# Kernel optimization log

Hardware: AMD Instinct MI355X
Metric: run time of the kernel (lower is better)

## Reference

```python
import jax, jax.numpy as jnp
import numpy as np

# --- static hash-grid config (matches tcnn HashGrid in the torch module) ---
DIM = 3
N_LEVELS = 16
F = 2                      # n_features_per_level
LOG2_T = 19
T = 1 << LOG2_T            # hashmap size per level
BASE_RES = 16
TARGET_RES = 2048
PLS = float(np.exp2(np.log2(TARGET_RES / BASE_RES) / (N_LEVELS - 1)))  # per_level_scale
SCALES = [BASE_RES * PLS ** l for l in range(N_LEVELS)]
PRIMES = np.array([1, 2654435761, 805459861], dtype=np.uint32)
# 8 corner offsets of the unit cube, shape [8, 3]
OFFS = np.stack(np.meshgrid(*([np.arange(2)] * DIM), indexing='ij'), -1).reshape(-1, DIM).astype(np.float32)


def _hash(idx_u32):
    # idx_u32: [..., 3] uint32 -> [...] uint32 index into table of size T (power of 2)
    h = idx_u32[..., 0] * jnp.uint32(PRIMES[0])
    h = h ^ (idx_u32[..., 1] * jnp.uint32(PRIMES[1]))
    h = h ^ (idx_u32[..., 2] * jnp.uint32(PRIMES[2]))
    return h & jnp.uint32(T - 1)


def hashgrid_encode(x, table):
    # x: [N, 3] in [0,1); table: [L, T, F] fp32
    outs = []
    offs = jnp.asarray(OFFS)                      # [8, 3]
    for l in range(N_LEVELS):
        pos = x * jnp.float32(SCALES[l])          # [N, 3]
        base = jnp.floor(pos)
        frac = pos - base                         # [N, 3]
        corner = base[:, None, :] + offs[None]    # [N, 8, 3]
        idx = corner.astype(jnp.uint32)
        h = _hash(idx)                            # [N, 8]
        feat = table[l][h]                        # [N, 8, F] (gather)
        # trilinear weights: prod over dims of frac or (1-frac)
        w = jnp.prod(jnp.where(offs[None] > 0.5, frac[:, None, :], 1.0 - frac[:, None, :]), axis=-1)  # [N, 8]
        outs.append(jnp.sum(w[..., None] * feat, axis=1))  # [N, F]
    return jnp.concatenate(outs, axis=-1)         # [N, L*F] = [N, 32]


def setup_inputs() -> dict:
    key = jax.random.key(0)
    ks = jax.random.split(key, 8)
    N = 1048576
    dim_in = N_LEVELS * F          # 32
    hid = 16                       # (16+15)//16*16
    dout = 16                      # grid_output_dim
    x = jax.random.uniform(ks[0], (N, DIM), dtype=jnp.float32)
    table = jax.random.uniform(ks[1], (N_LEVELS, T, F), dtype=jnp.float32, minval=-1e-4, maxval=1e-4)
    def lin(k, fi, fo):
        b = 1.0 / np.sqrt(fi)
        return jax.random.uniform(k, (fo, fi), dtype=jnp.float32, minval=-b, maxval=b)
    W0 = lin(ks[2], dim_in, hid); b0 = jnp.zeros((hid,), jnp.float32)
    W1 = lin(ks[3], hid, hid);    b1 = jnp.zeros((hid,), jnp.float32)
    W2 = lin(ks[4], hid, dout);   b2 = jnp.zeros((dout,), jnp.float32)
    return {"x": x, "table": table, "W0": W0, "b0": b0, "W1": W1, "b1": b1, "W2": W2, "b2": b2}


def reference(x, table, W0, b0, W1, b1, W2, b2):
    h = hashgrid_encode(x, table)                 # [N, 32]
    h = jax.nn.relu(h @ W0.T + b0)
    h = jax.nn.relu(h @ W1.T + b1)
    return h @ W2.T + b2                          # [N, 16]
```

## Files before the change

### kernel.cpp

```cpp
#include <hip/hip_runtime.h>
#include <math.h>

#define NLV 16
#define LOG2_T 19
#define T_SIZE (1u << LOG2_T)
#define T_MASK (T_SIZE - 1u)
#define P2 2654435761u
#define P3 805459861u
#define NBUCK 32768

typedef float vf2 __attribute__((ext_vector_type(2)));
typedef float vf4 __attribute__((ext_vector_type(4)));

struct Scales { float s[NLV]; };

__device__ __forceinline__ unsigned mpart(unsigned v) {
    v = (v | (v << 8)) & 0x100Fu;
    v = (v | (v << 4)) & 0x10C3u;
    v = (v | (v << 2)) & 0x1249u;
    return v;
}
__device__ __forceinline__ unsigned mkey(float px, float py, float pz) {
    unsigned cx = (unsigned)(px * 32.f); cx = cx > 31u ? 31u : cx;
    unsigned cy = (unsigned)(py * 32.f); cy = cy > 31u ? 31u : cy;
    unsigned cz = (unsigned)(pz * 32.f); cz = cz > 31u ? 31u : cz;
    return mpart(cx) | (mpart(cy) << 1) | (mpart(cz) << 2);
}

__global__ __launch_bounds__(256) void zero_hist_kernel(unsigned* hist) {
    int i = blockIdx.x * 256 + threadIdx.x;
    if (i < NBUCK) hist[i] = 0u;
}

__global__ __launch_bounds__(256) void hist_kernel(
    const float* __restrict__ x, unsigned* __restrict__ hist, int N)
{
    const int q = blockIdx.x * 256 + threadIdx.x;
    const int i0 = q * 4;
    if (i0 >= N) return;
    if (i0 + 3 < N) {
        const vf4 A = *(const vf4*)(x + 12 * (size_t)q);
        const vf4 B = *(const vf4*)(x + 12 * (size_t)q + 4);
        const vf4 C = *(const vf4*)(x + 12 * (size_t)q + 8);
        const float px[4] = {A[0], A[3], B[2], C[1]};
        const float py[4] = {A[1], B[0], B[3], C[2]};
        const float pz[4] = {A[2], B[1], C[0], C[3]};
        #pragma unroll
        for (int k = 0; k < 4; ++k) atomicAdd(&hist[mkey(px[k], py[k], pz[k])], 1u);
    } else {
        for (int i = i0; i < N; ++i)
            atomicAdd(&hist[mkey(x[3*(size_t)i], x[3*(size_t)i+1], x[3*(size_t)i+2])], 1u);
    }
}

__global__ __launch_bounds__(1024) void scan_kernel(unsigned* hist) {
    __shared__ unsigned tot[1024];
    const int t = threadIdx.x;
    const unsigned base = (unsigned)t * 32u;
    unsigned loc[32];
    unsigned s = 0;
    #pragma unroll
    for (int k = 0; k < 32; ++k) { loc[k] = s; s += hist[base + k]; }
    tot[t] = s;
    __syncthreads();
    for (int off = 1; off < 1024; off <<= 1) {
        unsigned u = (t >= off) ? tot[t - off] : 0u;
        __syncthreads();
        tot[t] += u;
        __syncthreads();
    }
    const unsigned excl = tot[t] - s;
    #pragma unroll
    for (int k = 0; k < 32; ++k) hist[base + k] = excl + loc[k];
}

__global__ __launch_bounds__(256) void scatter_kernel(
    const float* __restrict__ x, unsigned* __restrict__ cursor,
    vf4* __restrict__ xs, int* __restrict__ perm, int N)
{
    const int q = blockIdx.x * 256 + threadIdx.x;
    const int i0 = q * 4;
    if (i0 >= N) return;
    if (i0 + 3 < N) {
        const vf4 A = *(const vf4*)(x + 12 * (size_t)q);
        const vf4 B = *(const vf4*)(x + 12 * (size_t)q + 4);
        const vf4 C = *(const vf4*)(x + 12 * (size_t)q + 8);
        const float px[4] = {A[0], A[3], B[2], C[1]};
        const float py[4] = {A[1], B[0], B[3], C[2]};
        const float pz[4] = {A[2], B[1], C[0], C[3]};
        #pragma unroll
        for (int k = 0; k < 4; ++k) {
            const unsigned key = mkey(px[k], py[k], pz[k]);
            const unsigned pos = atomicAdd(&cursor[key], 1u);
            vf4 v; v[0] = px[k]; v[1] = py[k]; v[2] = pz[k]; v[3] = 0.f;
            xs[pos] = v;
            perm[pos] = i0 + k;
        }
    } else {
        for (int i = i0; i < N; ++i) {
            const float px = x[3*(size_t)i], py = x[3*(size_t)i+1], pz = x[3*(size_t)i+2];
            const unsigned key = mkey(px, py, pz);
            const unsigned pos = atomicAdd(&cursor[key], 1u);
            vf4 v; v[0] = px; v[1] = py; v[2] = pz; v[3] = 0.f;
            xs[pos] = v;
            perm[pos] = i;
        }
    }
}

__device__ __forceinline__ void enc_level(
    float px, float py, float pz, float s, const float* __restrict__ tl,
    float& f0, float& f1)
{
    const float fx = px * s, fy = py * s, fz = pz * s;
    const float bx = floorf(fx), by = floorf(fy), bz = floorf(fz);
    const float rx = fx - bx, ry = fy - by, rz = fz - bz;
    const unsigned ix0 = (unsigned)bx, iy0 = (unsigned)by, iz0 = (unsigned)bz;
    const unsigned hx0 = ix0,      hx1 = ix0 + 1u;
    const unsigned hy0 = iy0 * P2, hy1 = (iy0 + 1u) * P2;
    const unsigned hz0 = iz0 * P3, hz1 = (iz0 + 1u) * P3;
    const float wx0 = 1.f - rx, wy0 = 1.f - ry, wz0 = 1.f - rz;
    f0 = 0.f; f1 = 0.f;
    #pragma unroll
    for (int c = 0; c < 8; ++c) {
        unsigned h = ((c & 4) ? hx1 : hx0) ^ ((c & 2) ? hy1 : hy0) ^ ((c & 1) ? hz1 : hz0);
        h &= T_MASK;
        const vf2 f = *(const vf2*)(tl + 2u * (size_t)h);
        const float w = ((c & 4) ? rx : wx0) * ((c & 2) ? ry : wy0) * ((c & 1) ? rz : wz0);
        f0 += w * f[0];
        f1 += w * f[1];
    }
}

__global__ __launch_bounds__(256) void encode_coarse_kernel(
    const vf4* __restrict__ xs, const float* __restrict__ table,
    float* __restrict__ enc, int N, Scales sc)
{
    int i = blockIdx.x * 256 + threadIdx.x;
    if (i >= N) return;
    const vf4 p = xs[i];
    #pragma unroll
    for (int l = 0; l < 5; ++l) {
        float f0, f1;
        enc_level(p[0], p[1], p[2], sc.s[l], table + (size_t)l * T_SIZE * 2u, f0, f1);
        vf2 v; v[0] = f0; v[1] = f1;
        *(vf2*)(enc + ((size_t)l * N + i) * 2u) = v;
    }
}

__global__ __launch_bounds__(256) void encode_one_kernel(
    const vf4* __restrict__ xs, const float* __restrict__ tl, float s,
    float* __restrict__ encl, int N)
{
    const int i0 = blockIdx.x * 1024 + threadIdx.x;
    #pragma unroll
    for (int k = 0; k < 4; ++k) {
        const int i = i0 + k * 256;
        if (i < N) {
            const vf4 p = xs[i];
            float f0, f1;
            enc_level(p[0], p[1], p[2], s, tl, f0, f1);
            vf2 v; v[0] = f0; v[1] = f1;
            *(vf2*)(encl + (size_t)i * 2u) = v;
        }
    }
}

__global__ __launch_bounds__(256) void mlp_kernel(
    const float* __restrict__ enc, const int* __restrict__ perm,
    const float* __restrict__ W0, const float* __restrict__ b0,
    const float* __restrict__ W1, const float* __restrict__ b1,
    const float* __restrict__ W2, const float* __restrict__ b2,
    float* __restrict__ out, int N)
{
    __shared__ float st[512 * 17];
    const int base = blockIdx.x * 512;
    const int t = threadIdx.x;
    const int p0 = base + 2 * t;

    if (p0 < N) {
        float e[64];
        #pragma unroll
        for (int l = 0; l < NLV; ++l) {
            vf4 v = *(const vf4*)(enc + ((size_t)l * N + p0) * 2u);
            e[4*l+0] = v[0]; e[4*l+1] = v[1]; e[4*l+2] = v[2]; e[4*l+3] = v[3];
        }
        #pragma unroll
        for (int q = 0; q < 2; ++q) {
            if (q == 0 || p0 + 1 < N) {
                float a0[16];
                #pragma unroll
                for (int j = 0; j < 16; ++j) {
                    float s = b0[j];
                    #pragma unroll
                    for (int l = 0; l < NLV; ++l) {
                        s += e[4*l + 2*q + 0] * W0[j * 32 + 2*l + 0];
                        s += e[4*l + 2*q + 1] * W0[j * 32 + 2*l + 1];
                    }
                    a0[j] = fmaxf(s, 0.f);
                }
                float a1[16];
                #pragma unroll
                for (int j = 0; j < 16; ++j) {
                    float s = b1[j];
                    #pragma unroll
                    for (int k = 0; k < 16; ++k) s += a0[k] * W1[j * 16 + k];
                    a1[j] = fmaxf(s, 0.f);
                }
                const int row = 2 * t + q;
                #pragma unroll
                for (int j = 0; j < 16; ++j) {
                    float s = b2[j];
                    #pragma unroll
                    for (int k = 0; k < 16; ++k) s += a1[k] * W2[j * 16 + k];
                    st[row * 17 + j] = s;
                }
            }
        }
    }
    __syncthreads();

    const int c = t & 3;
    #pragma unroll
    for (int w = 0; w < 8; ++w) {
        const int p = (t >> 2) + w * 64;
        const int gi = base + p;
        if (gi < N) {
            const int dst = perm[gi];
            const vf4 v = *(const vf4*)&st[p * 17 + 4 * c];
            *(vf4*)(out + 16 * (size_t)dst + 4 * c) = v;
        }
    }
}

__global__ __launch_bounds__(256) void encode_coarse_unsorted_kernel(
    const float* __restrict__ x, const float* __restrict__ table,
    float* __restrict__ enc, int N, Scales sc)
{
    int i = blockIdx.x * 256 + threadIdx.x;
    if (i >= N) return;
    const float px = x[3 * (size_t)i + 0];
    const float py = x[3 * (size_t)i + 1];
    const float pz = x[3 * (size_t)i + 2];
    #pragma unroll
    for (int l = 0; l < 5; ++l) {
        float f0, f1;
        enc_level(px, py, pz, sc.s[l], table + (size_t)l * T_SIZE * 2u, f0, f1);
        vf2 v; v[0] = f0; v[1] = f1;
        *(vf2*)(enc + ((size_t)l * N + i) * 2u) = v;
    }
}
__global__ __launch_bounds__(256) void encode_one_unsorted_kernel(
    const float* __restrict__ x, const float* __restrict__ tl, float s,
    float* __restrict__ encl, int N)
{
    int i = blockIdx.x * 256 + threadIdx.x;
    if (i >= N) return;
    const float px = x[3 * (size_t)i + 0];
    const float py = x[3 * (size_t)i + 1];
    const float pz = x[3 * (size_t)i + 2];
    float f0, f1;
    enc_level(px, py, pz, s, tl, f0, f1);
    vf2 v; v[0] = f0; v[1] = f1;
    *(vf2*)(encl + (size_t)i * 2u) = v;
}
__global__ __launch_bounds__(256) void mlp_noperm_kernel(
    const float* __restrict__ enc,
    const float* __restrict__ W0, const float* __restrict__ b0,
    const float* __restrict__ W1, const float* __restrict__ b1,
    const float* __restrict__ W2, const float* __restrict__ b2,
    float* __restrict__ out, int N)
{
    int i = blockIdx.x * 256 + threadIdx.x;
    if (i >= N) return;
    float e[32];
    #pragma unroll
    for (int l = 0; l < NLV; ++l) {
        vf2 v = *(const vf2*)(enc + ((size_t)l * N + i) * 2u);
        e[2 * l + 0] = v[0];
        e[2 * l + 1] = v[1];
    }
    float a0[16];
    #pragma unroll
    for (int j = 0; j < 16; ++j) {
        float s = b0[j];
        #pragma unroll
        for (int k = 0; k < 32; ++k) s += e[k] * W0[j * 32 + k];
        a0[j] = fmaxf(s, 0.f);
    }
    float a1[16];
    #pragma unroll
    for (int j = 0; j < 16; ++j) {
        float s = b1[j];
        #pragma unroll
        for (int k = 0; k < 16; ++k) s += a0[k] * W1[j * 16 + k];
        a1[j] = fmaxf(s, 0.f);
    }
    #pragma unroll
    for (int j = 0; j < 16; ++j) {
        float s = b2[j];
        #pragma unroll
        for (int k = 0; k < 16; ++k) s += a1[k] * W2[j * 16 + k];
        out[16 * (size_t)i + j] = s;
    }
}
__global__ __launch_bounds__(256) void tcnn_fused_kernel(
    const float* __restrict__ x, const float* __restrict__ table,
    const float* __restrict__ W0, const float* __restrict__ b0,
    const float* __restrict__ W1, const float* __restrict__ b1,
    const float* __restrict__ W2, const float* __restrict__ b2,
    float* __restrict__ out, int N, Scales sc)
{
    int i = blockIdx.x * blockDim.x + threadIdx.x;
    if (i >= N) return;
    const float px = x[3 * (size_t)i + 0];
    const float py = x[3 * (size_t)i + 1];
    const float pz = x[3 * (size_t)i + 2];
    float e[32];
    #pragma unroll
    for (int l = 0; l < NLV; ++l) {
        float f0, f1;
        enc_level(px, py, pz, sc.s[l], table + (size_t)l * T_SIZE * 2u, f0, f1);
        e[2 * l] = f0; e[2 * l + 1] = f1;
    }
    float a0[16];
    #pragma unroll
    for (int j = 0; j < 16; ++j) {
        float s = b0[j];
        #pragma unroll
        for (int k = 0; k < 32; ++k) s += e[k] * W0[j * 32 + k];
        a0[j] = fmaxf(s, 0.f);
    }
    float a1[16];
    #pragma unroll
    for (int j = 0; j < 16; ++j) {
        float s = b1[j];
        #pragma unroll
        for (int k = 0; k < 16; ++k) s += a0[k] * W1[j * 16 + k];
        a1[j] = fmaxf(s, 0.f);
    }
    #pragma unroll
    for (int j = 0; j < 16; ++j) {
        float s = b2[j];
        #pragma unroll
        for (int k = 0; k < 16; ++k) s += a1[k] * W2[j * 16 + k];
        out[16 * (size_t)i + j] = s;
    }
}

extern "C" void kernel_launch(void* const* d_in, const int* in_sizes, int n_in,
                              void* d_out, int out_size, void* d_ws, size_t ws_size,
                              hipStream_t stream) {
    const float* x     = (const float*)d_in[0];
    const float* table = (const float*)d_in[1];
    const float* W0    = (const float*)d_in[2];
    const float* b0    = (const float*)d_in[3];
    const float* W1    = (const float*)d_in[4];
    const float* b1    = (const float*)d_in[5];
    const float* W2    = (const float*)d_in[6];
    const float* b2    = (const float*)d_in[7];
    float* out = (float*)d_out;

    const int N = in_sizes[0] / 3;

    Scales sc;
    const double pls = exp2(log2(2048.0 / 16.0) / 15.0);
    for (int l = 0; l < NLV; ++l) sc.s[l] = (float)(16.0 * pow(pls, (double)l));

    const int block = 256;
    const int grid = (N + block - 1) / block;

    const size_t encB  = (size_t)N * 2u * NLV * sizeof(float);
    const size_t xsB   = (size_t)N * sizeof(float) * 4u;
    const size_t permB = (size_t)N * sizeof(int);
    const size_t histB = (size_t)NBUCK * sizeof(unsigned);

    if (ws_size >= encB + xsB + permB + histB) {
        float*    enc  = (float*)d_ws;
        vf4*      xs   = (vf4*)((char*)d_ws + encB);
        int*      perm = (int*)((char*)d_ws + encB + xsB);
        unsigned* hist = (unsigned*)((char*)d_ws + encB + xsB + permB);

        const int gridQ = (N + 1023) / 1024;
        zero_hist_kernel<<<(NBUCK + 255) / 256, block, 0, stream>>>(hist);
        hist_kernel<<<gridQ, block, 0, stream>>>(x, hist, N);
        scan_kernel<<<1, 1024, 0, stream>>>(hist);
        scatter_kernel<<<gridQ, block, 0, stream>>>(x, hist, xs, perm, N);

        encode_coarse_kernel<<<grid, block, 0, stream>>>(xs, table, enc, N, sc);
        for (int l = 5; l < NLV; ++l) {
            encode_one_kernel<<<gridQ, block, 0, stream>>>(
                xs, table + (size_t)l * T_SIZE * 2u, sc.s[l],
                enc + (size_t)l * (size_t)N * 2u, N);
        }
        const int gridM = (N + 511) / 512;
        mlp_kernel<<<gridM, block, 0, stream>>>(enc, perm, W0, b0, W1, b1, W2, b2, out, N);
    } else if (ws_size >= encB) {
        float* enc = (float*)d_ws;
        encode_coarse_unsorted_kernel<<<grid, block, 0, stream>>>(x, table, enc, N, sc);
        for (int l = 5; l < NLV; ++l) {
            encode_one_unsorted_kernel<<<grid, block, 0, stream>>>(
                x, table + (size_t)l * T_SIZE * 2u, sc.s[l],
                enc + (size_t)l * (size_t)N * 2u, N);
        }
        mlp_noperm_kernel<<<grid, block, 0, stream>>>(enc, W0, b0, W1, b1, W2, b2, out, N);
    } else {
        tcnn_fused_kernel<<<grid, block, 0, stream>>>(x, table, W0, b0, W1, b1, W2, b2,
                                                      out, N, sc);
    }
}
```

Before: 533.1 us.

## Use atomic relaxed loads for fine-level gathers and restructure MLP to halve LDS

For hash levels 8 and up, table gathers now use relaxed agent-scope atomic 64-bit loads, apparently to change the cache policy and avoid polluting caches with random, low-reuse accesses. Separately, the MLP kernel processes its 512 points in two passes of 256. Each pass uses a half-size shared staging buffer and vectorized float2 dot products. This lowers LDS use and register pressure at the cost of an extra barrier and store phase. The atomic-load codegen may behave differently from plain loads on this hardware.

After: 554.4 us. 1.04x slower.

```diff
diff --git a/kernel.cpp b/kernel.cpp
--- a/kernel.cpp
+++ b/kernel.cpp
@@ -108,7 +108,8 @@
     }
 }
 
-__device__ __forceinline__ void enc_level(
+template<bool BYPASS>
+__device__ __forceinline__ void enc_level_t(
     float px, float py, float pz, float s, const float* __restrict__ tl,
     float& f0, float& f1)
 {
@@ -125,7 +126,15 @@
     for (int c = 0; c < 8; ++c) {
         unsigned h = ((c & 4) ? hx1 : hx0) ^ ((c & 2) ? hy1 : hy0) ^ ((c & 1) ? hz1 : hz0);
         h &= T_MASK;
-        const vf2 f = *(const vf2*)(tl + 2u * (size_t)h);
+        vf2 f;
+        if constexpr (BYPASS) {
+            unsigned long long u = __hip_atomic_load(
+                (const unsigned long long*)(tl + 2u * (size_t)h),
+                __ATOMIC_RELAXED, __HIP_MEMORY_SCOPE_AGENT);
+            union { unsigned long long u; vf2 f; } cv; cv.u = u; f = cv.f;
+        } else {
+            f = *(const vf2*)(tl + 2u * (size_t)h);
+        }
         const float w = ((c & 4) ? rx : wx0) * ((c & 2) ? ry : wy0) * ((c & 1) ? rz : wz0);
         f0 += w * f[0];
         f1 += w * f[1];
@@ -142,12 +151,13 @@
     #pragma unroll
     for (int l = 0; l < 5; ++l) {
         float f0, f1;
-        enc_level(p[0], p[1], p[2], sc.s[l], table + (size_t)l * T_SIZE * 2u, f0, f1);
+        enc_level_t<false>(p[0], p[1], p[2], sc.s[l], table + (size_t)l * T_SIZE * 2u, f0, f1);
         vf2 v; v[0] = f0; v[1] = f1;
         *(vf2*)(enc + ((size_t)l * N + i) * 2u) = v;
     }
 }
 
+template<bool BYPASS>
 __global__ __launch_bounds__(256) void encode_one_kernel(
     const vf4* __restrict__ xs, const float* __restrict__ tl, float s,
     float* __restrict__ encl, int N)
@@ -159,7 +169,7 @@
         if (i < N) {
             const vf4 p = xs[i];
             float f0, f1;
-            enc_level(p[0], p[1], p[2], s, tl, f0, f1);
+            enc_level_t<BYPASS>(p[0], p[1], p[2], s, tl, f0, f1);
             vf2 v; v[0] = f0; v[1] = f1;
             *(vf2*)(encl + (size_t)i * 2u) = v;
         }
@@ -173,62 +183,59 @@
     const float* __restrict__ W2, const float* __restrict__ b2,
     float* __restrict__ out, int N)
 {
-    __shared__ float st[512 * 17];
+    __shared__ float st[256 * 17];
     const int base = blockIdx.x * 512;
     const int t = threadIdx.x;
-    const int p0 = base + 2 * t;
-
-    if (p0 < N) {
-        float e[64];
-        #pragma unroll
-        for (int l = 0; l < NLV; ++l) {
-            vf4 v = *(const vf4*)(enc + ((size_t)l * N + p0) * 2u);
-            e[4*l+0] = v[0]; e[4*l+1] = v[1]; e[4*l+2] = v[2]; e[4*l+3] = v[3];
-        }
-        #pragma unroll
-        for (int q = 0; q < 2; ++q) {
-            if (q == 0 || p0 + 1 < N) {
-                float a0[16];
+
+    #pragma unroll
+    for (int q = 0; q < 2; ++q) {
+        if (q) __syncthreads();
+        const int i = base + q * 256 + t;
+        if (i < N) {
+            vf2 e2[16];
+            #pragma unroll
+            for (int l = 0; l < NLV; ++l)
+                e2[l] = *(const vf2*)(enc + ((size_t)l * N + i) * 2u);
+
+            vf2 a0v[8];
+            #pragma unroll
+            for (int j = 0; j < 16; ++j) {
+                vf2 acc = {0.f, 0.f};
                 #pragma unroll
-                for (int j = 0; j < 16; ++j) {
-                    float s = b0[j];
-                    #pragma unroll
-                    for (int l = 0; l < NLV; ++l) {
-                        s += e[4*l + 2*q + 0] * W0[j * 32 + 2*l + 0];
-                        s += e[4*l + 2*q + 1] * W0[j * 32 + 2*l + 1];
-                    }
-                    a0[j] = fmaxf(s, 0.f);
-                }
-                float a1[16];
+                for (int l = 0; l < 16; ++l)
+                    acc += e2[l] * *(const vf2*)(W0 + j * 32 + 2 * l);
+                a0v[j >> 1][j & 1] = fmaxf(b0[j] + acc[0] + acc[1], 0.f);
+            }
+            vf2 a1v[8];
+            #pragma unroll
+            for (int j = 0; j < 16; ++j) {
+                vf2 acc = {0.f, 0.f};
                 #pragma unroll
-                for (int j = 0; j < 16; ++j) {
-                    float s = b1[j];
-                    #pragma unroll
-                    for (int k = 0; k < 16; ++k) s += a0[k] * W1[j * 16 + k];
-                    a1[j] = fmaxf(s, 0.f);
-                }
-                const int row = 2 * t + q;
+                for (int k = 0; k < 8; ++k)
+                    acc += a0v[k] * *(const vf2*)(W1 + j * 16 + 2 * k);
+                a1v[j >> 1][j & 1] = fmaxf(b1[j] + acc[0] + acc[1], 0.f);
+            }
+            #pragma unroll
+            for (int j = 0; j < 16; ++j) {
+                vf2 acc = {0.f, 0.f};
                 #pragma unroll
-                for (int j = 0; j < 16; ++j) {
-                    float s = b2[j];
-                    #pragma unroll
-                    for (int k = 0; k < 16; ++k) s += a1[k] * W2[j * 16 + k];
-                    st[row * 17 + j] = s;
-                }
+                for (int k = 0; k < 8; ++k)
+                    acc += a1v[k] * *(const vf2*)(W2 + j * 16 + 2 * k);
+                st[t * 17 + j] = b2[j] + acc[0] + acc[1];
             }
         }
-    }
-    __syncthreads();
-
-    const int c = t & 3;
-    #pragma unroll
-    for (int w = 0; w < 8; ++w) {
-        const int p = (t >> 2) + w * 64;
-        const int gi = base + p;
-        if (gi < N) {
-            const int dst = perm[gi];
-            const vf4 v = *(const vf4*)&st[p * 17 + 4 * c];
-            *(vf4*)(out + 16 * (size_t)dst + 4 * c) = v;
+        __syncthreads();
+
+        const int c = t & 3;
+        #pragma unroll
+        for (int w = 0; w < 4; ++w) {
+            const int p = (t >> 2) + w * 64;
+            const int gi = base + q * 256 + p;
+            if (gi < N) {
+                const int dst = perm[gi];
+                const vf4 v = *(const vf4*)&st[p * 17 + 4 * c];
+                *(vf4*)(out + 16 * (size_t)dst + 4 * c) = v;
+            }
         }
     }
 }
@@ -245,7 +252,7 @@
     #pragma unroll
     for (int l = 0; l < 5; ++l) {
         float f0, f1;
-        enc_level(px, py, pz, sc.s[l], table + (size_t)l * T_SIZE * 2u, f0, f1);
+        enc_level_t<false>(px, py, pz, sc.s[l], table + (size_t)l * T_SIZE * 2u, f0, f1);
         vf2 v; v[0] = f0; v[1] = f1;
         *(vf2*)(enc + ((size_t)l * N + i) * 2u) = v;
     }
@@ -260,7 +267,7 @@
     const float py = x[3 * (size_t)i + 1];
     const float pz = x[3 * (size_t)i + 2];
     float f0, f1;
-    enc_level(px, py, pz, s, tl, f0, f1);
+    enc_level_t<false>(px, py, pz, s, tl, f0, f1);
     vf2 v; v[0] = f0; v[1] = f1;
     *(vf2*)(encl + (size_t)i * 2u) = v;
 }
@@ -320,7 +327,7 @@
     #pragma unroll
     for (int l = 0; l < NLV; ++l) {
         float f0, f1;
-        enc_level(px, py, pz, sc.s[l], table + (size_t)l * T_SIZE * 2u, f0, f1);
+        enc_level_t<false>(px, py, pz, sc.s[l], table + (size_t)l * T_SIZE * 2u, f0, f1);
         e[2 * l] = f0; e[2 * l + 1] = f1;
     }
     float a0[16];
@@ -388,8 +395,13 @@
         scatter_kernel<<<gridQ, block, 0, stream>>>(x, hist, xs, perm, N);
 
         encode_coarse_kernel<<<grid, block, 0, stream>>>(xs, table, enc, N, sc);
-        for (int l = 5; l < NLV; ++l) {
-            encode_one_kernel<<<gridQ, block, 0, stream>>>(
+        for (int l = 5; l < 8; ++l) {
+            encode_one_kernel<false><<<gridQ, block, 0, stream>>>(
+                xs, table + (size_t)l * T_SIZE * 2u, sc.s[l],
+                enc + (size_t)l * (size_t)N * 2u, N);
+        }
+        for (int l = 8; l < NLV; ++l) {
+            encode_one_kernel<true><<<gridQ, block, 0, stream>>>(
                 xs, table + (size_t)l * T_SIZE * 2u, sc.s[l],
                 enc + (size_t)l * (size_t)N * 2u, N);
         }
```
